# Kernel tuning notes

Measured on AMD Instinct MI355X. Metric: run time of the kernel, lower is better.

## Reference

```python
import jax, jax.numpy as jnp
import numpy as np

B, S, D = 4, 1024, 768
H = 12
K = 64            # max relative distance
R = 2 * K + 1     # number of relative buckets
DH = D // H       # per-head dim (k_dim and v_dim both == d_model here)


def setup_inputs() -> dict:
    key = jax.random.key(0)
    ks = jax.random.split(key, 14)
    s = 0.02
    return {
        "query": jax.random.normal(ks[0], (B, S, D), jnp.float32),
        "key":   jax.random.normal(ks[1], (B, S, D), jnp.float32),
        "value": jax.random.normal(ks[2], (B, S, D), jnp.float32),
        "WQ_w": jax.random.normal(ks[3], (D, D), jnp.float32) * s,
        "WQ_b": jnp.zeros((D,), jnp.float32),
        "WK_w": jax.random.normal(ks[4], (D, D), jnp.float32) * s,
        "WK_b": jnp.zeros((D,), jnp.float32),
        "WV_w": jax.random.normal(ks[5], (D, D), jnp.float32) * s,
        "WV_b": jnp.zeros((D,), jnp.float32),
        "WO_w": jax.random.normal(ks[6], (D, D), jnp.float32) * s,
        "WO_b": jnp.zeros((D,), jnp.float32),
        "embK": jax.random.normal(ks[7], (R, D), jnp.float32) * s,
        "embV": jax.random.normal(ks[8], (R, D), jnp.float32) * s,
    }


def _split_heads(x):  # [B,S,D] -> [B,H,S,DH]
    b, s, _ = x.shape
    return x.reshape(b, s, H, DH).transpose(0, 2, 1, 3)


def reference(query, key, value, WQ_w, WQ_b, WK_w, WK_b, WV_w, WV_b, WO_w, WO_b, embK, embV):
    Q = _split_heads(query @ WQ_w.T + WQ_b)   # [B,H,Sq,DH]
    Kt = _split_heads(key @ WK_w.T + WK_b)    # [B,H,Sk,DH]
    V = _split_heads(value @ WV_w.T + WV_b)   # [B,H,Sk,DH]

    Sq, Sk = Q.shape[2], Kt.shape[2]
    # clipped relative position bucket index, matching get_relative_matrix
    idx = jnp.clip(jnp.arange(Sk)[None, :] - jnp.arange(Sq)[:, None], -K, K) + K  # [Sq,Sk]
    qrows = jnp.arange(Sq)[:, None]

    # content scores
    qk = jnp.einsum('bhqd,bhkd->bhqk', Q, Kt)
    # relative-K scores: project Q onto all R buckets, then gather per (q,k).
    # Mathematically identical to einsum('bhqd,hqkd->bhqk', Q, gather(embK)).
    embK_h = embK.reshape(R, H, DH)
    rel_all = jnp.einsum('bhqd,rhd->bhqr', Q, embK_h)        # [B,H,Sq,R]
    rel_scores = rel_all[:, :, qrows, idx]                   # [B,H,Sq,Sk]

    scores = (qk + rel_scores) / jnp.sqrt(jnp.asarray(DH, jnp.float32))
    attn = jax.nn.softmax(scores, axis=-1)                   # [B,H,Sq,Sk]

    out = jnp.einsum('bhqk,bhkv->bhqv', attn, V)             # [B,H,Sq,DH]
    # relative-V: scatter attention mass into R buckets per query, then one GEMM.
    w = jnp.zeros((B, H, Sq, R), attn.dtype).at[:, :, qrows, idx].add(attn)
    embV_h = embV.reshape(R, H, DH)
    out = out + jnp.einsum('bhqr,rhv->bhqv', w, embV_h)

    out = out.transpose(0, 2, 1, 3).reshape(B, Sq, D)        # merge heads
    out = out @ WO_w.T + WO_b                                 # (dropout p=0 is identity)
    return out, attn
```

## Files before the change

### kernel.cpp

```cpp
#include <hip/hip_runtime.h>

typedef _Float16 f16;
typedef _Float16 f16x4 __attribute__((ext_vector_type(4)));
typedef _Float16 f16x8 __attribute__((ext_vector_type(8)));
typedef float    f32x4 __attribute__((ext_vector_type(4)));

#define DEV static __device__ __forceinline__

DEV f32x4 mfma16(f16x8 a, f16x8 b, f32x4 c) {
    return __builtin_amdgcn_mfma_f32_16x16x32_f16(a, b, c, 0, 0, 0);
}

DEV void gload16(const f16* g, f16* l) {
    __builtin_amdgcn_global_load_lds(
        (const __attribute__((address_space(1))) unsigned int*)g,
        (__attribute__((address_space(3))) unsigned int*)l,
        16, 0, 0);
}


struct ConvArgs {
    const float* src[8];
    f16*         dst[8];
};

__global__ __launch_bounds__(256) void k_convert(ConvArgs a) {
    const int seg[9] = {0, 786432, 1572864, 2359296, 2506752, 2654208,
                        2801664, 2949120, 2973888};
    for (int i = blockIdx.x * 256 + threadIdx.x; i < 2973888; i += gridDim.x * 256) {
        int s = 0;
        while (i >= seg[s + 1]) s++;
        const int j = i - seg[s];
        const float4 v = ((const float4*)a.src[s])[j];
        f16x4 o;
        o[0] = (f16)v.x; o[1] = (f16)v.y; o[2] = (f16)v.z; o[3] = (f16)v.w;
        ((f16x4*)a.dst[s])[j] = o;
    }
}

__global__ __launch_bounds__(256) void k_embvt(const float* __restrict__ embV,
                                               f16* __restrict__ dst) {
    const int idx = blockIdx.x * 256 + threadIdx.x;
    if (idx >= 12 * 64 * 160) return;
    const int r  = idx % 160;
    const int dh = (idx / 160) % 64;
    const int h  = idx / (160 * 64);
    float v = 0.f;
    if (r < 129) v = embV[r * 768 + h * 64 + dh];
    dst[idx] = (f16)v;
}

#define GEMM_TILE_BODY(X, W)                                                   \
    const int tid = threadIdx.x;                                               \
    const int w = tid >> 6, l = tid & 63, quad = l >> 4, l16 = l & 15;         \
    const int wr = w >> 1, wc = w & 1;                                         \
    const int rl = l >> 2, cc = l & 3;                                         \
    const int csrc = (cc ^ ((rl ^ (rl >> 2)) & 3)) * 8;                        \
    const f16* gA = (X) + (size_t)(m0 + w * 32 + rl) * 768 + csrc;             \
    const f16* gB = (W) + (size_t)(n0 + w * 32 + rl) * 768 + csrc;             \
    f16* lA0 = As + (w * 32) * 32;                                             \
    f16* lA1 = As + (w * 32 + 16) * 32;                                        \
    f16* lB0 = Bs + (w * 32) * 32;                                             \
    f16* lB1 = Bs + (w * 32 + 16) * 32;                                        \
    const int xsw = (quad ^ ((l16 ^ (l16 >> 2)) & 3)) * 8;                     \
    f32x4 acc[4][4] = {};                                                      \
    for (int k0 = 0; k0 < 768; k0 += 32) {                                     \
        __syncthreads();                                                       \
        gload16(gA + k0, lA0);                                                 \
        gload16(gA + k0 + 16 * 768, lA1);                                      \
        gload16(gB + k0, lB0);                                                 \
        gload16(gB + k0 + 16 * 768, lB1);                                      \
        __syncthreads();                                                       \
        f16x8 af[4], bf[4];                                                    \
        _Pragma("unroll") for (int i = 0; i < 4; i++)                          \
            af[i] = *(const f16x8*)(As + (wr * 64 + i * 16 + l16) * 32 + xsw); \
        _Pragma("unroll") for (int i = 0; i < 4; i++)                          \
            bf[i] = *(const f16x8*)(Bs + (wc * 64 + i * 16 + l16) * 32 + xsw); \
        _Pragma("unroll") for (int i = 0; i < 4; i++)                          \
            _Pragma("unroll") for (int j = 0; j < 4; j++)                      \
                acc[i][j] = mfma16(af[i], bf[j], acc[i][j]);                   \
    }

__global__ __launch_bounds__(256) void k_gemm_qkv(
    const f16* __restrict__ xq, const f16* __restrict__ xk, const f16* __restrict__ xv,
    const f16* __restrict__ wq, const f16* __restrict__ wk, const f16* __restrict__ wv,
    const float* __restrict__ bq, const float* __restrict__ bk, const float* __restrict__ bv,
    f16* __restrict__ Qh, f16* __restrict__ Kh, f16* __restrict__ Vt) {
    __shared__ __align__(16) f16 As[128 * 32];
    __shared__ __align__(16) f16 Bs[128 * 32];

    const int t  = blockIdx.y / 6;
    const int n0 = (blockIdx.y % 6) * 128;
    const int m0 = blockIdx.x * 128;
    const f16*   X    = (t == 0) ? xq : (t == 1) ? xk : xv;
    const f16*   W    = (t == 0) ? wq : (t == 1) ? wk : wv;
    const float* bias = (t == 0) ? bq : (t == 1) ? bk : bv;

    GEMM_TILE_BODY(X, W)

#pragma unroll
    for (int j = 0; j < 4; j++) {
        const int   nj = n0 + wc * 64 + j * 16 + l16;
        const float bb = bias[nj];
        const int   h = nj >> 6, dh = nj & 63;
#pragma unroll
        for (int i = 0; i < 4; i++) {
            const int mb = m0 + wr * 64 + i * 16 + quad * 4;
            const int b = mb >> 10, s = mb & 1023;
            if (t < 2) {
                f16* dst = (t == 0) ? Qh : Kh;
                const int base = ((b * 12 + h) * 1024 + s) * 64 + dh;
#pragma unroll
                for (int r = 0; r < 4; r++)
                    dst[base + r * 64] = (f16)(acc[i][j][r] + bb);
            } else {
                f16x4 pk;
#pragma unroll
                for (int r = 0; r < 4; r++) pk[r] = (f16)(acc[i][j][r] + bb);
                *(f16x4*)(Vt + ((b * 12 + h) * 64 + dh) * 1024 + s) = pk;
            }
        }
    }
}

__global__ __launch_bounds__(256) void k_gemm_out(
    const f16* __restrict__ Xin, const f16* __restrict__ Win,
    const float* __restrict__ bias, float* __restrict__ out) {
    __shared__ __align__(16) f16 As[128 * 32];
    __shared__ __align__(16) f16 Bs[128 * 32];

    const int n0 = blockIdx.y * 128;
    const int m0 = blockIdx.x * 128;

    GEMM_TILE_BODY(Xin, Win)

#pragma unroll
    for (int j = 0; j < 4; j++) {
        const int   nj = n0 + wc * 64 + j * 16 + l16;
        const float bb = bias[nj];
#pragma unroll
        for (int i = 0; i < 4; i++) {
            const int mb = m0 + wr * 64 + i * 16 + quad * 4;
#pragma unroll
            for (int r = 0; r < 4; r++)
                out[(size_t)(mb + r) * 768 + nj] = acc[i][j][r] + bb;
        }
    }
}

constexpr int SCP = 1032;

__global__ __launch_bounds__(256) void k_attn(
    const f16* __restrict__ Qh, const f16* __restrict__ Kh, const f16* __restrict__ Vt,
    const f16* __restrict__ embK, const f16* __restrict__ embVt,
    float* __restrict__ attn, f16* __restrict__ ctx) {
    __shared__ __align__(16) f16 sc[16 * SCP];
    __shared__ __align__(16) f16 relw[16 * 160];
    __shared__ float red[3][4][16];
    __shared__ float invs[16], tl0[16], tl1[16];

    const int qt = blockIdx.x, bh = blockIdx.y;
    const int b = bh / 12, h = bh % 12;
    const int q0 = qt * 16;
    const int tid = threadIdx.x;
    const int w = tid >> 6, l = tid & 63, quad = l >> 4, l16 = l & 15;

    const f16* Qb = Qh + (bh * 1024 + q0) * 64;
    const f16* Kb = Kh + bh * 1024 * 64;
    const f16* Vb = Vt + bh * 64 * 1024;

    const f16x8 qa0 = *(const f16x8*)(Qb + l16 * 64 + quad * 8);
    const f16x8 qa1 = *(const f16x8*)(Qb + l16 * 64 + 32 + quad * 8);

    for (int nf = w; nf < 9; nf += 4) {
        const int r0 = nf * 16;
        int rr = r0 + l16; if (rr > 128) rr = 128;
        const f16x8 b0 = *(const f16x8*)(embK + rr * 768 + h * 64 + quad * 8);
        const f16x8 b1 = *(const f16x8*)(embK + rr * 768 + h * 64 + 32 + quad * 8);
        f32x4 a = {};
        a = mfma16(qa0, b0, a);
        a = mfma16(qa1, b1, a);
#pragma unroll
        for (int r = 0; r < 4; r++)
            relw[(quad * 4 + r) * 160 + r0 + l16] = (f16)a[r];
    }
    __syncthreads();

    float rs[4] = {0.f, 0.f, 0.f, 0.f};
    float rt0[4] = {0.f, 0.f, 0.f, 0.f};
    float rt1[4] = {0.f, 0.f, 0.f, 0.f};
    for (int nf = 0; nf < 16; nf++) {
        const int kc = w * 256 + nf * 16;
        const f16x8 b0 = *(const f16x8*)(Kb + (kc + l16) * 64 + quad * 8);
        const f16x8 b1 = *(const f16x8*)(Kb + (kc + l16) * 64 + 32 + quad * 8);
        f32x4 a = {};
        a = mfma16(qa0, b0, a);
        a = mfma16(qa1, b1, a);
        const int kg = kc + l16;
#pragma unroll
        for (int r = 0; r < 4; r++) {
            const int row = quad * 4 + r;
            const int qg = q0 + row;
            int d = kg - qg;
            d = (d < -64) ? -64 : (d > 64) ? 64 : d;
            const float s = (a[r] + (float)relw[row * 160 + d + 64]) * 0.125f;
            const float e = __expf(s);
            sc[row * SCP + kg] = (f16)e;
            rs[r] += e;
            rt0[r] += (kg <= qg - 64) ? e : 0.f;
            rt1[r] += (kg >= qg + 64) ? e : 0.f;
        }
    }
#pragma unroll
    for (int r = 0; r < 4; r++)
        for (int o = 1; o < 16; o <<= 1) {
            rs[r]  += __shfl_xor(rs[r], o);
            rt0[r] += __shfl_xor(rt0[r], o);
            rt1[r] += __shfl_xor(rt1[r], o);
        }
    if (l16 == 0) {
#pragma unroll
        for (int r = 0; r < 4; r++) {
            red[0][w][quad * 4 + r] = rs[r];
            red[1][w][quad * 4 + r] = rt0[r];
            red[2][w][quad * 4 + r] = rt1[r];
        }
    }
    __syncthreads();
    if (tid < 16) {
        const float s = red[0][0][tid] + red[0][1][tid] + red[0][2][tid] + red[0][3][tid];
        invs[tid] = 1.f / s;
        tl0[tid] = red[1][0][tid] + red[1][1][tid] + red[1][2][tid] + red[1][3][tid];
        tl1[tid] = red[2][0][tid] + red[2][1][tid] + red[2][2][tid] + red[2][3][tid];
    }
    __syncthreads();

    {
        float* ab = attn + ((long)bh * 1024 + q0) * 1024;
#pragma unroll
        for (int rr = 0; rr < 4; rr++) {
            const int row = w * 4 + rr;
            const float inv = invs[row];
            const f16* p = sc + row * SCP;
            float* o = ab + (long)row * 1024;
#pragma unroll
            for (int jj = 0; jj < 4; jj++) {
                const int c = jj * 256 + l * 4;
                const f16x4 v = *(const f16x4*)(p + c);
                *(float4*)(o + c) = make_float4((float)v[0] * inv, (float)v[1] * inv,
                                                (float)v[2] * inv, (float)v[3] * inv);
            }
        }
    }
    for (int idx = tid; idx < 16 * 160; idx += 256) {
        const int row = idx / 160, r = idx - row * 160;
        float v = 0.f;
        if (r == 0) v = tl0[row];
        else if (r == 128) v = tl1[row];
        else if (r < 128) {
            const int col = q0 + row + r - 64;
            if (col >= 0 && col < 1024) v = (float)sc[row * SCP + col];
        }
        relw[idx] = (f16)v;
    }
    __syncthreads();

    {
        f32x4 a = {};
        const f16* vrow = Vb + (w * 16 + l16) * 1024;
        for (int ks = 0; ks < 32; ks++) {
            const f16x8 af = *(const f16x8*)(sc + l16 * SCP + ks * 32 + quad * 8);
            const f16x8 bf = *(const f16x8*)(vrow + ks * 32 + quad * 8);
            a = mfma16(af, bf, a);
        }
        const f16* erow = embVt + (h * 64 + w * 16 + l16) * 160;
#pragma unroll
        for (int ks = 0; ks < 5; ks++) {
            const f16x8 af = *(const f16x8*)(relw + l16 * 160 + ks * 32 + quad * 8);
            const f16x8 bf = *(const f16x8*)(erow + ks * 32 + quad * 8);
            a = mfma16(af, bf, a);
        }
#pragma unroll
        for (int r = 0; r < 4; r++) {
            const int row = quad * 4 + r;
            const int qg = q0 + row;
            ctx[(b * 1024 + qg) * 768 + h * 64 + w * 16 + l16] = (f16)(a[r] * invs[row]);
        }
    }
}

extern "C" void kernel_launch(void* const* d_in, const int* in_sizes, int n_in,
                              void* d_out, int out_size, void* d_ws, size_t ws_size,
                              hipStream_t stream) {
    const float* q_in = (const float*)d_in[0];
    const float* k_in = (const float*)d_in[1];
    const float* v_in = (const float*)d_in[2];
    const float* WQw  = (const float*)d_in[3];
    const float* WQb  = (const float*)d_in[4];
    const float* WKw  = (const float*)d_in[5];
    const float* WKb  = (const float*)d_in[6];
    const float* WVw  = (const float*)d_in[7];
    const float* WVb  = (const float*)d_in[8];
    const float* WOw  = (const float*)d_in[9];
    const float* WOb  = (const float*)d_in[10];
    const float* embK = (const float*)d_in[11];
    const float* embV = (const float*)d_in[12];

    char*  ws  = (char*)d_ws;
    size_t off = 0;
    auto nxt = [&](size_t n) {
        char* p = ws + off;
        off += (n + 255) & ~(size_t)255;
        return p;
    };
    f16* qb    = (f16*)nxt(3145728 * 2);
    f16* kb    = (f16*)nxt(3145728 * 2);
    f16* vb    = (f16*)nxt(3145728 * 2);
    f16* Wqb   = (f16*)nxt(589824 * 2);
    f16* Wkb   = (f16*)nxt(589824 * 2);
    f16* Wvb   = (f16*)nxt(589824 * 2);
    f16* Wob   = (f16*)nxt(589824 * 2);
    f16* embKb = (f16*)nxt(99072 * 2);
    f16* embVt = (f16*)nxt(122880 * 2);
    f16* Qh    = (f16*)nxt(3145728 * 2);
    f16* Kh    = (f16*)nxt(3145728 * 2);
    f16* Vt    = (f16*)nxt(3145728 * 2);
    f16* ctx   = (f16*)nxt(3145728 * 2);
    (void)ws_size; (void)in_sizes; (void)n_in; (void)out_size;

    ConvArgs ca;
    ca.src[0] = q_in; ca.src[1] = k_in; ca.src[2] = v_in;
    ca.src[3] = WQw;  ca.src[4] = WKw;  ca.src[5] = WVw;
    ca.src[6] = WOw;  ca.src[7] = embK;
    ca.dst[0] = qb;   ca.dst[1] = kb;   ca.dst[2] = vb;
    ca.dst[3] = Wqb;  ca.dst[4] = Wkb;  ca.dst[5] = Wvb;
    ca.dst[6] = Wob;  ca.dst[7] = embKb;

    k_convert<<<dim3(2048), dim3(256), 0, stream>>>(ca);
    k_embvt<<<dim3(480), dim3(256), 0, stream>>>(embV, embVt);
    k_gemm_qkv<<<dim3(32, 18), dim3(256), 0, stream>>>(
        qb, kb, vb, Wqb, Wkb, Wvb, WQb, WKb, WVb, Qh, Kh, Vt);
    float* attn = (float*)d_out + 3145728;
    k_attn<<<dim3(64, 48), dim3(256), 0, stream>>>(Qh, Kh, Vt, embKb, embVt, attn, ctx);
    k_gemm_out<<<dim3(32, 6), dim3(256), 0, stream>>>(ctx, Wob, WOb, (float*)d_out);
}
```

Before: 398.2 us.

## Fuse activation fp16 conversion into QKV GEMM, add V transpose kernel, retile output GEMM

The QKV GEMM now reads the fp32 activations directly and converts them to fp16 in registers before storing to LDS, so the separate conversion pass over the activations and its extra buffer traffic are gone. V is written head-major and transposed afterwards by a new LDS-tiled kernel, which replaces the scattered 4-element transposed stores. The output GEMM switches to 64-row tiles, doubling the number of blocks for better CU occupancy. In the attention kernel the relative-bias handling gets fast paths for key tiles that lie entirely outside the clip window, and the relw row stride is padded to 168. In exchange, the A-operand loads in the QKV GEMM become synchronous register loads instead of direct-to-LDS loads, and there is an extra kernel launch.

After: 403.9 us. Within noise of the previous version (+1.4%).

```diff
diff --git a/kernel.cpp b/kernel.cpp
--- a/kernel.cpp
+++ b/kernel.cpp
@@ -20,14 +20,13 @@
 
 
 struct ConvArgs {
-    const float* src[8];
-    f16*         dst[8];
+    const float* src[5];
+    f16*         dst[5];
 };
 
-__global__ __launch_bounds__(256) void k_convert(ConvArgs a) {
-    const int seg[9] = {0, 786432, 1572864, 2359296, 2506752, 2654208,
-                        2801664, 2949120, 2973888};
-    for (int i = blockIdx.x * 256 + threadIdx.x; i < 2973888; i += gridDim.x * 256) {
+__global__ __launch_bounds__(256) void k_convw(ConvArgs a) {
+    const int seg[6] = {0, 147456, 294912, 442368, 589824, 614592};
+    for (int i = blockIdx.x * 256 + threadIdx.x; i < 614592; i += gridDim.x * 256) {
         int s = 0;
         while (i >= seg[s + 1]) s++;
         const int j = i - seg[s];
@@ -50,54 +49,67 @@
     dst[idx] = (f16)v;
 }
 
-#define GEMM_TILE_BODY(X, W)                                                   \
-    const int tid = threadIdx.x;                                               \
-    const int w = tid >> 6, l = tid & 63, quad = l >> 4, l16 = l & 15;         \
-    const int wr = w >> 1, wc = w & 1;                                         \
-    const int rl = l >> 2, cc = l & 3;                                         \
-    const int csrc = (cc ^ ((rl ^ (rl >> 2)) & 3)) * 8;                        \
-    const f16* gA = (X) + (size_t)(m0 + w * 32 + rl) * 768 + csrc;             \
-    const f16* gB = (W) + (size_t)(n0 + w * 32 + rl) * 768 + csrc;             \
-    f16* lA0 = As + (w * 32) * 32;                                             \
-    f16* lA1 = As + (w * 32 + 16) * 32;                                        \
-    f16* lB0 = Bs + (w * 32) * 32;                                             \
-    f16* lB1 = Bs + (w * 32 + 16) * 32;                                        \
-    const int xsw = (quad ^ ((l16 ^ (l16 >> 2)) & 3)) * 8;                     \
-    f32x4 acc[4][4] = {};                                                      \
-    for (int k0 = 0; k0 < 768; k0 += 32) {                                     \
-        __syncthreads();                                                       \
-        gload16(gA + k0, lA0);                                                 \
-        gload16(gA + k0 + 16 * 768, lA1);                                      \
-        gload16(gB + k0, lB0);                                                 \
-        gload16(gB + k0 + 16 * 768, lB1);                                      \
-        __syncthreads();                                                       \
-        f16x8 af[4], bf[4];                                                    \
-        _Pragma("unroll") for (int i = 0; i < 4; i++)                          \
-            af[i] = *(const f16x8*)(As + (wr * 64 + i * 16 + l16) * 32 + xsw); \
-        _Pragma("unroll") for (int i = 0; i < 4; i++)                          \
-            bf[i] = *(const f16x8*)(Bs + (wc * 64 + i * 16 + l16) * 32 + xsw); \
-        _Pragma("unroll") for (int i = 0; i < 4; i++)                          \
-            _Pragma("unroll") for (int j = 0; j < 4; j++)                      \
-                acc[i][j] = mfma16(af[i], bf[j], acc[i][j]);                   \
-    }
-
 __global__ __launch_bounds__(256) void k_gemm_qkv(
-    const f16* __restrict__ xq, const f16* __restrict__ xk, const f16* __restrict__ xv,
+    const float* __restrict__ xq, const float* __restrict__ xk, const float* __restrict__ xv,
     const f16* __restrict__ wq, const f16* __restrict__ wk, const f16* __restrict__ wv,
     const float* __restrict__ bq, const float* __restrict__ bk, const float* __restrict__ bv,
-    f16* __restrict__ Qh, f16* __restrict__ Kh, f16* __restrict__ Vt) {
+    f16* __restrict__ Qh, f16* __restrict__ Kh, f16* __restrict__ Vh) {
     __shared__ __align__(16) f16 As[128 * 32];
     __shared__ __align__(16) f16 Bs[128 * 32];
 
     const int t  = blockIdx.y / 6;
     const int n0 = (blockIdx.y % 6) * 128;
     const int m0 = blockIdx.x * 128;
-    const f16*   X    = (t == 0) ? xq : (t == 1) ? xk : xv;
+    const float* X    = (t == 0) ? xq : (t == 1) ? xk : xv;
     const f16*   W    = (t == 0) ? wq : (t == 1) ? wk : wv;
     const float* bias = (t == 0) ? bq : (t == 1) ? bk : bv;
 
-    GEMM_TILE_BODY(X, W)
-
+    const int tid = threadIdx.x;
+    const int w = tid >> 6, l = tid & 63, quad = l >> 4, l16 = l & 15;
+    const int wr = w >> 1, wc = w & 1;
+    const int rl = l >> 2, cc = l & 3;
+    const int csrc = (cc ^ ((rl ^ (rl >> 2)) & 3)) * 8;
+    const float* gA = X + (size_t)(m0 + w * 32 + rl) * 768 + csrc;
+    const f16*   gB = W + (size_t)(n0 + w * 32 + rl) * 768 + csrc;
+    f16* lA0 = As + (w * 32) * 32;
+    f16* lA1 = As + (w * 32 + 16) * 32;
+    f16* lB0 = Bs + (w * 32) * 32;
+    f16* lB1 = Bs + (w * 32 + 16) * 32;
+    const int xsw = (quad ^ ((l16 ^ (l16 >> 2)) & 3)) * 8;
+
+    f32x4 acc[4][4] = {};
+
+    for (int k0 = 0; k0 < 768; k0 += 32) {
+        const float4 a00 = *(const float4*)(gA + k0);
+        const float4 a01 = *(const float4*)(gA + k0 + 4);
+        const float4 a10 = *(const float4*)(gA + k0 + 16 * 768);
+        const float4 a11 = *(const float4*)(gA + k0 + 16 * 768 + 4);
+        __syncthreads();
+        f16x8 pa0, pa1;
+        pa0[0] = (f16)a00.x; pa0[1] = (f16)a00.y; pa0[2] = (f16)a00.z; pa0[3] = (f16)a00.w;
+        pa0[4] = (f16)a01.x; pa0[5] = (f16)a01.y; pa0[6] = (f16)a01.z; pa0[7] = (f16)a01.w;
+        pa1[0] = (f16)a10.x; pa1[1] = (f16)a10.y; pa1[2] = (f16)a10.z; pa1[3] = (f16)a10.w;
+        pa1[4] = (f16)a11.x; pa1[5] = (f16)a11.y; pa1[6] = (f16)a11.z; pa1[7] = (f16)a11.w;
+        ((f16x8*)lA0)[l] = pa0;
+        ((f16x8*)lA1)[l] = pa1;
+        gload16(gB + k0, lB0);
+        gload16(gB + k0 + 16 * 768, lB1);
+        __syncthreads();
+        f16x8 af[4], bf[4];
+#pragma unroll
+        for (int i = 0; i < 4; i++)
+            af[i] = *(const f16x8*)(As + (wr * 64 + i * 16 + l16) * 32 + xsw);
+#pragma unroll
+        for (int i = 0; i < 4; i++)
+            bf[i] = *(const f16x8*)(Bs + (wc * 64 + i * 16 + l16) * 32 + xsw);
+#pragma unroll
+        for (int i = 0; i < 4; i++)
+#pragma unroll
+            for (int j = 0; j < 4; j++)
+                acc[i][j] = mfma16(af[i], bf[j], acc[i][j]);
+    }
+
+    f16* dst = (t == 0) ? Qh : (t == 1) ? Kh : Vh;
 #pragma unroll
     for (int j = 0; j < 4; j++) {
         const int   nj = n0 + wc * 64 + j * 16 + l16;
@@ -107,40 +119,84 @@
         for (int i = 0; i < 4; i++) {
             const int mb = m0 + wr * 64 + i * 16 + quad * 4;
             const int b = mb >> 10, s = mb & 1023;
-            if (t < 2) {
-                f16* dst = (t == 0) ? Qh : Kh;
-                const int base = ((b * 12 + h) * 1024 + s) * 64 + dh;
-#pragma unroll
-                for (int r = 0; r < 4; r++)
-                    dst[base + r * 64] = (f16)(acc[i][j][r] + bb);
-            } else {
-                f16x4 pk;
-#pragma unroll
-                for (int r = 0; r < 4; r++) pk[r] = (f16)(acc[i][j][r] + bb);
-                *(f16x4*)(Vt + ((b * 12 + h) * 64 + dh) * 1024 + s) = pk;
-            }
-        }
-    }
+            const int base = ((b * 12 + h) * 1024 + s) * 64 + dh;
+#pragma unroll
+            for (int r = 0; r < 4; r++)
+                dst[base + r * 64] = (f16)(acc[i][j][r] + bb);
+        }
+    }
+}
+
+__global__ __launch_bounds__(256) void k_vt(const f16* __restrict__ Vh,
+                                            f16* __restrict__ Vt) {
+    __shared__ __align__(16) f16 ld[64 * 72];
+    const int s0 = blockIdx.x * 64, bh = blockIdx.y;
+    const int tid = threadIdx.x;
+    const int sr = tid >> 2;
+    const int ch = tid & 3;
+    const f16* src = Vh + ((size_t)bh * 1024 + s0 + sr) * 64 + ch * 16;
+    const f16x8 v0 = *(const f16x8*)(src);
+    const f16x8 v1 = *(const f16x8*)(src + 8);
+#pragma unroll
+    for (int c = 0; c < 8; c++) ld[(ch * 16 + c) * 72 + sr] = v0[c];
+#pragma unroll
+    for (int c = 0; c < 8; c++) ld[(ch * 16 + 8 + c) * 72 + sr] = v1[c];
+    __syncthreads();
+    const int dh = tid >> 2;
+    f16* dst = Vt + ((size_t)bh * 64 + dh) * 1024 + s0 + ch * 16;
+    *(f16x8*)(dst)     = *(const f16x8*)(ld + dh * 72 + ch * 16);
+    *(f16x8*)(dst + 8) = *(const f16x8*)(ld + dh * 72 + ch * 16 + 8);
 }
 
 __global__ __launch_bounds__(256) void k_gemm_out(
     const f16* __restrict__ Xin, const f16* __restrict__ Win,
     const float* __restrict__ bias, float* __restrict__ out) {
-    __shared__ __align__(16) f16 As[128 * 32];
+    __shared__ __align__(16) f16 As[64 * 32];
     __shared__ __align__(16) f16 Bs[128 * 32];
 
+    const int m0 = blockIdx.x * 64;
     const int n0 = blockIdx.y * 128;
-    const int m0 = blockIdx.x * 128;
-
-    GEMM_TILE_BODY(Xin, Win)
+    const int tid = threadIdx.x;
+    const int w = tid >> 6, l = tid & 63, quad = l >> 4, l16 = l & 15;
+    const int mh = w & 1, nh = w >> 1;
+    const int rl = l >> 2, cc = l & 3;
+    const int csrc = (cc ^ ((rl ^ (rl >> 2)) & 3)) * 8;
+    const f16* gA = Xin + (size_t)(m0 + w * 16 + rl) * 768 + csrc;
+    const f16* gB = Win + (size_t)(n0 + w * 32 + rl) * 768 + csrc;
+    f16* lA  = As + (w * 16) * 32;
+    f16* lB0 = Bs + (w * 32) * 32;
+    f16* lB1 = Bs + (w * 32 + 16) * 32;
+    const int xsw = (quad ^ ((l16 ^ (l16 >> 2)) & 3)) * 8;
+
+    f32x4 acc[2][4] = {};
+
+    for (int k0 = 0; k0 < 768; k0 += 32) {
+        __syncthreads();
+        gload16(gA + k0, lA);
+        gload16(gB + k0, lB0);
+        gload16(gB + k0 + 16 * 768, lB1);
+        __syncthreads();
+        f16x8 af[2], bf[4];
+#pragma unroll
+        for (int i = 0; i < 2; i++)
+            af[i] = *(const f16x8*)(As + (mh * 32 + i * 16 + l16) * 32 + xsw);
+#pragma unroll
+        for (int j = 0; j < 4; j++)
+            bf[j] = *(const f16x8*)(Bs + (nh * 64 + j * 16 + l16) * 32 + xsw);
+#pragma unroll
+        for (int i = 0; i < 2; i++)
+#pragma unroll
+            for (int j = 0; j < 4; j++)
+                acc[i][j] = mfma16(af[i], bf[j], acc[i][j]);
+    }
 
 #pragma unroll
     for (int j = 0; j < 4; j++) {
-        const int   nj = n0 + wc * 64 + j * 16 + l16;
+        const int   nj = n0 + nh * 64 + j * 16 + l16;
         const float bb = bias[nj];
 #pragma unroll
-        for (int i = 0; i < 4; i++) {
-            const int mb = m0 + wr * 64 + i * 16 + quad * 4;
+        for (int i = 0; i < 2; i++) {
+            const int mb = m0 + mh * 32 + i * 16 + quad * 4;
 #pragma unroll
             for (int r = 0; r < 4; r++)
                 out[(size_t)(mb + r) * 768 + nj] = acc[i][j][r] + bb;
@@ -149,13 +205,14 @@
 }
 
 constexpr int SCP = 1032;
+constexpr int RST = 168;
 
 __global__ __launch_bounds__(256) void k_attn(
     const f16* __restrict__ Qh, const f16* __restrict__ Kh, const f16* __restrict__ Vt,
     const f16* __restrict__ embK, const f16* __restrict__ embVt,
     float* __restrict__ attn, f16* __restrict__ ctx) {
     __shared__ __align__(16) f16 sc[16 * SCP];
-    __shared__ __align__(16) f16 relw[16 * 160];
+    __shared__ __align__(16) f16 relw[16 * RST];
     __shared__ float red[3][4][16];
     __shared__ float invs[16], tl0[16], tl1[16];
 
@@ -182,11 +239,18 @@
         a = mfma16(qa1, b1, a);
 #pragma unroll
         for (int r = 0; r < 4; r++)
-            relw[(quad * 4 + r) * 160 + r0 + l16] = (f16)a[r];
+            relw[(quad * 4 + r) * RST + r0 + l16] = (f16)a[r];
     }
     __syncthreads();
 
-    float rs[4] = {0.f, 0.f, 0.f, 0.f};
+    float rlo[4], rhi[4];
+#pragma unroll
+    for (int r = 0; r < 4; r++) {
+        rlo[r] = (float)relw[(quad * 4 + r) * RST + 0];
+        rhi[r] = (float)relw[(quad * 4 + r) * RST + 128];
+    }
+
+    float rs[4]  = {0.f, 0.f, 0.f, 0.f};
     float rt0[4] = {0.f, 0.f, 0.f, 0.f};
     float rt1[4] = {0.f, 0.f, 0.f, 0.f};
     for (int nf = 0; nf < 16; nf++) {
@@ -197,18 +261,35 @@
         a = mfma16(qa0, b0, a);
         a = mfma16(qa1, b1, a);
         const int kg = kc + l16;
-#pragma unroll
-        for (int r = 0; r < 4; r++) {
-            const int row = quad * 4 + r;
-            const int qg = q0 + row;
-            int d = kg - qg;
-            d = (d < -64) ? -64 : (d > 64) ? 64 : d;
-            const float s = (a[r] + (float)relw[row * 160 + d + 64]) * 0.125f;
-            const float e = __expf(s);
-            sc[row * SCP + kg] = (f16)e;
-            rs[r] += e;
-            rt0[r] += (kg <= qg - 64) ? e : 0.f;
-            rt1[r] += (kg >= qg + 64) ? e : 0.f;
+        if (kc + 80 <= q0) {
+#pragma unroll
+            for (int r = 0; r < 4; r++) {
+                const int row = quad * 4 + r;
+                const float e = __expf((a[r] + rlo[r]) * 0.125f);
+                sc[row * SCP + kg] = (f16)e;
+                rs[r] += e; rt0[r] += e;
+            }
+        } else if (kc >= q0 + 80) {
+#pragma unroll
+            for (int r = 0; r < 4; r++) {
+                const int row = quad * 4 + r;
+                const float e = __expf((a[r] + rhi[r]) * 0.125f);
+                sc[row * SCP + kg] = (f16)e;
+                rs[r] += e; rt1[r] += e;
+            }
+        } else {
+#pragma unroll
+            for (int r = 0; r < 4; r++) {
+                const int row = quad * 4 + r;
+                const int qg = q0 + row;
+                int d = kg - qg;
+                d = (d < -64) ? -64 : (d > 64) ? 64 : d;
+                const float e = __expf((a[r] + (float)relw[row * RST + d + 64]) * 0.125f);
+                sc[row * SCP + kg] = (f16)e;
+                rs[r] += e;
+                rt0[r] += (kg <= qg - 64) ? e : 0.f;
+                rt1[r] += (kg >= qg + 64) ? e : 0.f;
+            }
         }
     }
 #pragma unroll
@@ -261,7 +342,7 @@
             const int col = q0 + row + r - 64;
             if (col >= 0 && col < 1024) v = (float)sc[row * SCP + col];
         }
-        relw[idx] = (f16)v;
+        relw[row * RST + r] = (f16)v;
     }
     __syncthreads();
 
@@ -276,7 +357,7 @@
         const f16* erow = embVt + (h * 64 + w * 16 + l16) * 160;
 #pragma unroll
         for (int ks = 0; ks < 5; ks++) {
-            const f16x8 af = *(const f16x8*)(relw + l16 * 160 + ks * 32 + quad * 8);
+            const f16x8 af = *(const f16x8*)(relw + l16 * RST + ks * 32 + quad * 8);
             const f16x8 bf = *(const f16x8*)(erow + ks * 32 + quad * 8);
             a = mfma16(af, bf, a);
         }
@@ -313,9 +394,6 @@
         off += (n + 255) & ~(size_t)255;
         return p;
     };
-    f16* qb    = (f16*)nxt(3145728 * 2);
-    f16* kb    = (f16*)nxt(3145728 * 2);
-    f16* vb    = (f16*)nxt(3145728 * 2);
     f16* Wqb   = (f16*)nxt(589824 * 2);
     f16* Wkb   = (f16*)nxt(589824 * 2);
     f16* Wvb   = (f16*)nxt(589824 * 2);
@@ -324,23 +402,21 @@
     f16* embVt = (f16*)nxt(122880 * 2);
     f16* Qh    = (f16*)nxt(3145728 * 2);
     f16* Kh    = (f16*)nxt(3145728 * 2);
+    f16* Vh    = (f16*)nxt(3145728 * 2);
     f16* Vt    = (f16*)nxt(3145728 * 2);
     f16* ctx   = (f16*)nxt(3145728 * 2);
     (void)ws_size; (void)in_sizes; (void)n_in; (void)out_size;
 
     ConvArgs ca;
-    ca.src[0] = q_in; ca.src[1] = k_in; ca.src[2] = v_in;
-    ca.src[3] = WQw;  ca.src[4] = WKw;  ca.src[5] = WVw;
-    ca.src[6] = WOw;  ca.src[7] = embK;
-    ca.dst[0] = qb;   ca.dst[1] = kb;   ca.dst[2] = vb;
-    ca.dst[3] = Wqb;  ca.dst[4] = Wkb;  ca.dst[5] = Wvb;
-    ca.dst[6] = Wob;  ca.dst[7] = embKb;
-
-    k_convert<<<dim3(2048), dim3(256), 0, stream>>>(ca);
+    ca.src[0] = WQw; ca.src[1] = WKw; ca.src[2] = WVw; ca.src[3] = WOw; ca.src[4] = embK;
+    ca.dst[0] = Wqb; ca.dst[1] = Wkb; ca.dst[2] = Wvb; ca.dst[3] = Wob; ca.dst[4] = embKb;
+
+    k_convw<<<dim3(1200), dim3(256), 0, stream>>>(ca);
     k_embvt<<<dim3(480), dim3(256), 0, stream>>>(embV, embVt);
     k_gemm_qkv<<<dim3(32, 18), dim3(256), 0, stream>>>(
-        qb, kb, vb, Wqb, Wkb, Wvb, WQb, WKb, WVb, Qh, Kh, Vt);
+        q_in, k_in, v_in, Wqb, Wkb, Wvb, WQb, WKb, WVb, Qh, Kh, Vh);
+    k_vt<<<dim3(16, 48), dim3(256), 0, stream>>>(Vh, Vt);
     float* attn = (float*)d_out + 3145728;
     k_attn<<<dim3(64, 48), dim3(256), 0, stream>>>(Qh, Kh, Vt, embKb, embVt, attn, ctx);
-    k_gemm_out<<<dim3(32, 6), dim3(256), 0, stream>>>(ctx, Wob, WOb, (float*)d_out);
-}
+    k_gemm_out<<<dim3(64, 6), dim3(256), 0, stream>>>(ctx, Wob, WOb, (float*)d_out);
+}
```
